# Kernel tuning notes

Hardware: AMD Instinct MI355X
Metric: run time of the kernel (lower is better)

The kernel has to match this reference:

```python
import jax, jax.numpy as jnp
import numpy as np

B, N, D_IN, D_HID, D_EDGE = 4, 256, 256, 256, 64


def setup_inputs() -> dict:
    key = jax.random.key(0)
    ks = jax.random.split(key, 8)
    s_in = 1.0 / np.sqrt(D_IN)
    s_h2 = 1.0 / np.sqrt(2 * D_HID)
    s_h = 1.0 / np.sqrt(D_HID)
    return {
        "x": jax.random.normal(ks[0], (B, N, D_IN), jnp.float32),
        "W_in": jax.random.uniform(ks[1], (D_HID, D_IN), jnp.float32, -s_in, s_in),
        "b_in": jax.random.uniform(ks[2], (D_HID,), jnp.float32, -s_in, s_in),
        "W1": jax.random.uniform(ks[3], (D_HID, 2 * D_HID), jnp.float32, -s_h2, s_h2),
        "b1": jax.random.uniform(ks[4], (D_HID,), jnp.float32, -s_h2, s_h2),
        "W2": jax.random.uniform(ks[5], (D_EDGE, D_HID), jnp.float32, -s_h, s_h),
        "b2": jax.random.uniform(ks[6], (D_EDGE,), jnp.float32, -s_h, s_h),
    }


def reference(x, W_in, b_in, W1, b1, W2, b2):
    # in_proj: [B,N,d_in] -> [B,N,h]
    h = jnp.einsum("bnd,hd->bnh", x, W_in) + b_in
    # cat([h_i, h_j]) @ W1 == h_i @ Wa + h_j @ Wb with W1 = [Wa | Wb].
    # Precompute the two N x h projections, then broadcast-add over the pair grid
    # instead of materializing the [B,N,N,2h] concat (same math, fused form).
    Wa, Wb = W1[:, :D_HID], W1[:, D_HID:]
    pa = jnp.einsum("bnh,gh->bng", h, Wa)  # [B,N,h]
    pb = jnp.einsum("bnh,gh->bng", h, Wb)  # [B,N,h]
    z = pa[:, :, None, :] + pb[:, None, :, :] + b1  # [B,N,N,h]
    z = z * jax.nn.sigmoid(z)  # Swish
    return jnp.einsum("bijh,eh->bije", z, W2) + b2  # [B,N,N,d_edge]
```

## Files before the change

kernel.cpp:

```cpp
#include <hip/hip_runtime.h>

#define DIN 256
#define DHID 256
#define DEDGE 64
#define GS 68

typedef float f32x4 __attribute__((ext_vector_type(4)));
typedef short s16x8 __attribute__((ext_vector_type(8)));
typedef unsigned int u32x4 __attribute__((ext_vector_type(4)));

__device__ __forceinline__ unsigned int cvtpk(float lo, float hi) {
    unsigned int r;
    asm("v_cvt_pk_bf16_f32 %0, %1, %2" : "=v"(r) : "v"(lo), "v"(hi));
    return r;
}

__global__ __launch_bounds__(256) void k_xh(
    const float* __restrict__ x, const float* __restrict__ Win,
    float* __restrict__ hp, const float* __restrict__ W2, s16x8* __restrict__ W2f)
{
    const int tid = threadIdx.x;
    if (blockIdx.z == 4) {
        if (tid < 32) {
            const int f = (((blockIdx.x << 2) + blockIdx.y) << 5) + tid;
            const int l15f = f & 15, qf = (f >> 4) & 3, ebf = (f >> 6) & 3, k0f = f >> 8;
            const int row = (ebf << 4) + l15f;
            const int col = (k0f << 5) + (qf << 3);
            const f32x4 w0 = *reinterpret_cast<const f32x4*>(&W2[row * DHID + col]);
            const f32x4 w1 = *reinterpret_cast<const f32x4*>(&W2[row * DHID + col + 4]);
            u32x4 wp;
            wp[0] = cvtpk(w0[0], w0[1]); wp[1] = cvtpk(w0[2], w0[3]);
            wp[2] = cvtpk(w1[0], w1[1]); wp[3] = cvtpk(w1[2], w1[3]);
            W2f[f] = __builtin_bit_cast(s16x8, wp);
        }
        return;
    }

    __shared__ float as[64 * GS];
    __shared__ float ws[64 * GS];
    const int m0 = blockIdx.x << 6, n0 = blockIdx.y << 6, k0 = blockIdx.z << 6;
    const int rr = tid >> 4;
    const int kk = (tid & 15) << 2;

#pragma unroll
    for (int it = 0; it < 4; ++it) {
        const int row = rr + (it << 4);
        *reinterpret_cast<f32x4*>(&as[row * GS + kk]) =
            *reinterpret_cast<const f32x4*>(&x[(m0 + row) * DIN + k0 + kk]);
        *reinterpret_cast<f32x4*>(&ws[row * GS + kk]) =
            *reinterpret_cast<const f32x4*>(&Win[(n0 + row) * DIN + k0 + kk]);
    }
    __syncthreads();

    const int tx = tid & 15, ty = tid >> 4;
    float acc[4][4] = {};
    for (int k = 0; k < 64; k += 4) {
        f32x4 av[4], wv[4];
#pragma unroll
        for (int r = 0; r < 4; ++r)
            av[r] = *reinterpret_cast<const f32x4*>(&as[(ty + (r << 4)) * GS + k]);
#pragma unroll
        for (int c = 0; c < 4; ++c)
            wv[c] = *reinterpret_cast<const f32x4*>(&ws[(tx + (c << 4)) * GS + k]);
#pragma unroll
        for (int r = 0; r < 4; ++r)
#pragma unroll
            for (int c = 0; c < 4; ++c)
                acc[r][c] += av[r][0]*wv[c][0] + av[r][1]*wv[c][1]
                           + av[r][2]*wv[c][2] + av[r][3]*wv[c][3];
    }
    float* dst = hp + ((size_t)blockIdx.z << 18);
#pragma unroll
    for (int r = 0; r < 4; ++r)
#pragma unroll
        for (int c = 0; c < 4; ++c)
            dst[(m0 + ty + (r << 4)) * DHID + n0 + tx + (c << 4)] = acc[r][c];
}

__global__ __launch_bounds__(256) void k_pab(
    const float* __restrict__ hp, const float* __restrict__ W1,
    const float* __restrict__ bin, float* __restrict__ pap, float* __restrict__ pbp)
{
    __shared__ float as[64 * GS];
    __shared__ float ws[64 * GS];
    const int m0 = blockIdx.x << 6;
    const int half = blockIdx.y >> 2;
    const int n0 = (blockIdx.y & 3) << 6;
    const int kc = blockIdx.z;
    const int tid = threadIdx.x;
    const int rr = tid >> 4, kk = (tid & 15) << 2;
    const int tx = tid & 15, ty = tid >> 4;

    float acc[4][4] = {};
    for (int kt = 0; kt < 2; ++kt) {
        const int k0 = (kc << 7) + (kt << 6);
        if (kt) __syncthreads();
#pragma unroll
        for (int it = 0; it < 4; ++it) {
            const int row = rr + (it << 4);
            const int aoff = (m0 + row) * DHID + k0 + kk;
            f32x4 av = *reinterpret_cast<const f32x4*>(&hp[aoff]);
            av += *reinterpret_cast<const f32x4*>(&hp[aoff + (1 << 18)]);
            av += *reinterpret_cast<const f32x4*>(&hp[aoff + (2 << 18)]);
            av += *reinterpret_cast<const f32x4*>(&hp[aoff + (3 << 18)]);
            av += *reinterpret_cast<const f32x4*>(&bin[k0 + kk]);
            *reinterpret_cast<f32x4*>(&as[row * GS + kk]) = av;
            *reinterpret_cast<f32x4*>(&ws[row * GS + kk]) =
                *reinterpret_cast<const f32x4*>(&W1[(n0 + row) * 512 + (half << 8) + k0 + kk]);
        }
        __syncthreads();

        for (int k = 0; k < 64; k += 4) {
            f32x4 av[4], wv[4];
#pragma unroll
            for (int r = 0; r < 4; ++r)
                av[r] = *reinterpret_cast<const f32x4*>(&as[(ty + (r << 4)) * GS + k]);
#pragma unroll
            for (int c = 0; c < 4; ++c)
                wv[c] = *reinterpret_cast<const f32x4*>(&ws[(tx + (c << 4)) * GS + k]);
#pragma unroll
            for (int r = 0; r < 4; ++r)
#pragma unroll
                for (int c = 0; c < 4; ++c)
                    acc[r][c] += av[r][0]*wv[c][0] + av[r][1]*wv[c][1]
                               + av[r][2]*wv[c][2] + av[r][3]*wv[c][3];
        }
    }
    float* dst = (half ? pbp : pap) + ((size_t)kc << 18);
#pragma unroll
    for (int r = 0; r < 4; ++r)
#pragma unroll
        for (int c = 0; c < 4; ++c)
            dst[(m0 + ty + (r << 4)) * DHID + n0 + tx + (c << 4)] = acc[r][c];
}

__global__ __launch_bounds__(256) void k_out(
    const float* __restrict__ pap, const float* __restrict__ pbp,
    const float* __restrict__ b1, const s16x8* __restrict__ W2f,
    const float* __restrict__ b2, float* __restrict__ out)
{
    __shared__ s16x8 w2s[2048];
    __shared__ float pab1[4][DHID];

    const int jb = blockIdx.x, i0 = blockIdx.y << 2, b = blockIdx.z;
    const int tid = threadIdx.x;

    {
        const float b1v = b1[tid];
#pragma unroll
        for (int ii = 0; ii < 4; ++ii) {
            const int off = (((b << 8) + i0 + ii) << 8) + tid;
            pab1[ii][tid] = pap[off] + pap[off + (1 << 18)] + b1v;
        }
    }
#pragma unroll
    for (int it = 0; it < 8; ++it)
        w2s[tid + (it << 8)] = W2f[tid + (it << 8)];
    __syncthreads();

    const int lane = tid & 63, wave = tid >> 6, quad = lane >> 4, l15 = lane & 15;
    const int j0 = (jb << 6) + (wave << 4);
    const int pboff = (((b << 8) + (j0 + l15)) << 8);
    const float* pbq0 = pbp + pboff;
    const float* pbq1 = pbp + (1 << 18) + pboff;

    f32x4 acc[4][4];
#pragma unroll
    for (int ii = 0; ii < 4; ++ii)
#pragma unroll
        for (int eb = 0; eb < 4; ++eb) acc[ii][eb] = (f32x4){0.f, 0.f, 0.f, 0.f};

    float b2v[4];
#pragma unroll
    for (int eb = 0; eb < 4; ++eb) b2v[eb] = b2[(eb << 4) + l15];

    for (int k0 = 0; k0 < 8; ++k0) {
        const int g = (k0 << 5) + (quad << 3);
        const f32x4 p0 = *reinterpret_cast<const f32x4*>(pbq0 + g)
                       + *reinterpret_cast<const f32x4*>(pbq1 + g);
        const f32x4 p1 = *reinterpret_cast<const f32x4*>(pbq0 + g + 4)
                       + *reinterpret_cast<const f32x4*>(pbq1 + g + 4);

        s16x8 bfrag[4];
#pragma unroll
        for (int eb = 0; eb < 4; ++eb)
            bfrag[eb] = w2s[((k0 << 2) + eb) * 64 + lane];

#pragma unroll
        for (int ii = 0; ii < 4; ++ii) {
            const f32x4 q0 = *reinterpret_cast<const f32x4*>(&pab1[ii][g]);
            const f32x4 q1 = *reinterpret_cast<const f32x4*>(&pab1[ii][g + 4]);
            float s[8];
#pragma unroll
            for (int jj = 0; jj < 4; ++jj) {
                const float z0 = q0[jj] + p0[jj];
                const float z1 = q1[jj] + p1[jj];
                const float e0 = __expf(-z0);
                const float e1 = __expf(-z1);
                s[jj]     = z0 * __builtin_amdgcn_rcpf(1.0f + e0);
                s[4 + jj] = z1 * __builtin_amdgcn_rcpf(1.0f + e1);
            }
            u32x4 ap;
            ap[0] = cvtpk(s[0], s[1]); ap[1] = cvtpk(s[2], s[3]);
            ap[2] = cvtpk(s[4], s[5]); ap[3] = cvtpk(s[6], s[7]);
            const s16x8 a = __builtin_bit_cast(s16x8, ap);
#pragma unroll
            for (int eb = 0; eb < 4; ++eb)
                acc[ii][eb] = __builtin_amdgcn_mfma_f32_16x16x32_bf16(a, bfrag[eb], acc[ii][eb], 0, 0, 0);
        }
    }

#pragma unroll
    for (int ii = 0; ii < 4; ++ii) {
        const int obase = (((((b << 8) + i0 + ii) << 8) + j0 + (quad << 2)) << 6) + l15;
#pragma unroll
        for (int eb = 0; eb < 4; ++eb) {
#pragma unroll
            for (int r = 0; r < 4; ++r)
                __builtin_nontemporal_store(acc[ii][eb][r] + b2v[eb],
                                            &out[obase + (r << 6) + (eb << 4)]);
        }
    }
}

extern "C" void kernel_launch(void* const* d_in, const int* in_sizes, int n_in,
                              void* d_out, int out_size, void* d_ws, size_t ws_size,
                              hipStream_t stream) {
    const float* x = 0; const float* Win = 0; const float* bin = 0;
    const float* W1 = 0; const float* b1 = 0; const float* W2 = 0; const float* b2 = 0;
    for (int idx = 0; idx < n_in; ++idx) {
        const int s = in_sizes[idx];
        if (s == 262144) x = (const float*)d_in[idx];
        else if (s == 131072) W1 = (const float*)d_in[idx];
        else if (s == 65536) Win = (const float*)d_in[idx];
        else if (s == 16384) W2 = (const float*)d_in[idx];
        else if (s == 64) b2 = (const float*)d_in[idx];
        else if (s == 256) { if (!bin) bin = (const float*)d_in[idx]; else b1 = (const float*)d_in[idx]; }
    }

    float* ws  = (float*)d_ws;
    float* hp  = ws;
    float* pap = hp + (4 << 18);
    float* pbp = pap + (2 << 18);
    float* w2f = pbp + (2 << 18);

    hipLaunchKernelGGL(k_xh,  dim3(16, 4, 5), dim3(256), 0, stream, x, Win, hp, W2, (s16x8*)w2f);
    hipLaunchKernelGGL(k_pab, dim3(16, 8, 2), dim3(256), 0, stream, hp, W1, bin, pap, pbp);
    hipLaunchKernelGGL(k_out, dim3(4, 64, 4), dim3(256), 0, stream,
                       pap, pbp, b1, (const s16x8*)w2f, b2, (float*)d_out);
}
```

Measured before the change: 125.8 us.

## Use split-bf16 MFMA for the pa/pb projection GEMM in k_pab

Replaces the scalar fp32 FMA tile GEMM in k_pab with bf16 MFMA 16x16x32 instructions. Operands are split into hi and lo bf16 parts and three MFMAs per tile (hi*hi, hi*lo, lo*hi) recover near-fp32 accuracy. Shared memory now holds four bf16 arrays with padded stride, and the K loop is processed in a single staged chunk. This trades extra conversion work and a small accuracy loss for matrix-core throughput on a kernel that is a small part of total time.

Result: faster. 120.9 us (-3.9%).

```diff
diff --git a/kernel.cpp b/kernel.cpp
--- a/kernel.cpp
+++ b/kernel.cpp
@@ -4,9 +4,11 @@
 #define DHID 256
 #define DEDGE 64
 #define GS 68
+#define BS 136
 
 typedef float f32x4 __attribute__((ext_vector_type(4)));
 typedef short s16x8 __attribute__((ext_vector_type(8)));
+typedef unsigned int u32x2 __attribute__((ext_vector_type(2)));
 typedef unsigned int u32x4 __attribute__((ext_vector_type(4)));
 
 __device__ __forceinline__ unsigned int cvtpk(float lo, float hi) {
@@ -81,57 +83,83 @@
     const float* __restrict__ hp, const float* __restrict__ W1,
     const float* __restrict__ bin, float* __restrict__ pap, float* __restrict__ pbp)
 {
-    __shared__ float as[64 * GS];
-    __shared__ float ws[64 * GS];
+    __shared__ unsigned short Ahi[64 * BS], Alo[64 * BS];
+    __shared__ unsigned short Bhi[64 * BS], Blo[64 * BS];
     const int m0 = blockIdx.x << 6;
     const int half = blockIdx.y >> 2;
     const int n0 = (blockIdx.y & 3) << 6;
     const int kc = blockIdx.z;
     const int tid = threadIdx.x;
-    const int rr = tid >> 4, kk = (tid & 15) << 2;
-    const int tx = tid & 15, ty = tid >> 4;
-
-    float acc[4][4] = {};
-    for (int kt = 0; kt < 2; ++kt) {
-        const int k0 = (kc << 7) + (kt << 6);
-        if (kt) __syncthreads();
-#pragma unroll
-        for (int it = 0; it < 4; ++it) {
-            const int row = rr + (it << 4);
-            const int aoff = (m0 + row) * DHID + k0 + kk;
-            f32x4 av = *reinterpret_cast<const f32x4*>(&hp[aoff]);
-            av += *reinterpret_cast<const f32x4*>(&hp[aoff + (1 << 18)]);
-            av += *reinterpret_cast<const f32x4*>(&hp[aoff + (2 << 18)]);
-            av += *reinterpret_cast<const f32x4*>(&hp[aoff + (3 << 18)]);
-            av += *reinterpret_cast<const f32x4*>(&bin[k0 + kk]);
-            *reinterpret_cast<f32x4*>(&as[row * GS + kk]) = av;
-            *reinterpret_cast<f32x4*>(&ws[row * GS + kk]) =
-                *reinterpret_cast<const f32x4*>(&W1[(n0 + row) * 512 + (half << 8) + k0 + kk]);
-        }
-        __syncthreads();
-
-        for (int k = 0; k < 64; k += 4) {
-            f32x4 av[4], wv[4];
-#pragma unroll
-            for (int r = 0; r < 4; ++r)
-                av[r] = *reinterpret_cast<const f32x4*>(&as[(ty + (r << 4)) * GS + k]);
-#pragma unroll
-            for (int c = 0; c < 4; ++c)
-                wv[c] = *reinterpret_cast<const f32x4*>(&ws[(tx + (c << 4)) * GS + k]);
-#pragma unroll
-            for (int r = 0; r < 4; ++r)
-#pragma unroll
-                for (int c = 0; c < 4; ++c)
-                    acc[r][c] += av[r][0]*wv[c][0] + av[r][1]*wv[c][1]
-                               + av[r][2]*wv[c][2] + av[r][3]*wv[c][3];
-        }
-    }
+    const int k0 = kc << 7;
+
+    const int srow = tid >> 2, sc0 = (tid & 3) << 2;
+    {
+        const float* hpA = hp + (m0 + srow) * DHID + k0 + sc0;
+        const float* w1B = W1 + (n0 + srow) * 512 + (half << 8) + k0 + sc0;
+        const float* binp = bin + k0 + sc0;
+#pragma unroll
+        for (int g2 = 0; g2 < 8; ++g2) {
+            const int c = g2 << 4;
+            f32x4 av = *reinterpret_cast<const f32x4*>(hpA + c);
+            av += *reinterpret_cast<const f32x4*>(hpA + c + (1 << 18));
+            av += *reinterpret_cast<const f32x4*>(hpA + c + (2 << 18));
+            av += *reinterpret_cast<const f32x4*>(hpA + c + (3 << 18));
+            av += *reinterpret_cast<const f32x4*>(binp + c);
+            unsigned int ah0 = cvtpk(av[0], av[1]), ah1 = cvtpk(av[2], av[3]);
+            f32x4 hf;
+            hf[0] = __builtin_bit_cast(float, ah0 << 16);
+            hf[1] = __builtin_bit_cast(float, ah0 & 0xffff0000u);
+            hf[2] = __builtin_bit_cast(float, ah1 << 16);
+            hf[3] = __builtin_bit_cast(float, ah1 & 0xffff0000u);
+            const f32x4 alo = av - hf;
+            const int la = srow * BS + sc0 + c;
+            *reinterpret_cast<u32x2*>(&Ahi[la]) = (u32x2){ah0, ah1};
+            *reinterpret_cast<u32x2*>(&Alo[la]) = (u32x2){cvtpk(alo[0], alo[1]), cvtpk(alo[2], alo[3])};
+
+            f32x4 bv = *reinterpret_cast<const f32x4*>(w1B + c);
+            unsigned int bh0 = cvtpk(bv[0], bv[1]), bh1 = cvtpk(bv[2], bv[3]);
+            f32x4 bf;
+            bf[0] = __builtin_bit_cast(float, bh0 << 16);
+            bf[1] = __builtin_bit_cast(float, bh0 & 0xffff0000u);
+            bf[2] = __builtin_bit_cast(float, bh1 << 16);
+            bf[3] = __builtin_bit_cast(float, bh1 & 0xffff0000u);
+            const f32x4 blo = bv - bf;
+            *reinterpret_cast<u32x2*>(&Bhi[la]) = (u32x2){bh0, bh1};
+            *reinterpret_cast<u32x2*>(&Blo[la]) = (u32x2){cvtpk(blo[0], blo[1]), cvtpk(blo[2], blo[3])};
+        }
+    }
+    __syncthreads();
+
+    const int lane = tid & 63, wave = tid >> 6, quad = lane >> 4, l15 = lane & 15;
+    const int arow = (wave << 4) + l15;
+
+    f32x4 acc[4];
+#pragma unroll
+    for (int nb = 0; nb < 4; ++nb) acc[nb] = (f32x4){0.f, 0.f, 0.f, 0.f};
+
+#pragma unroll
+    for (int ks = 0; ks < 4; ++ks) {
+        const int kcol = (ks << 5) + (quad << 3);
+        const s16x8 ahi = *reinterpret_cast<const s16x8*>(&Ahi[arow * BS + kcol]);
+        const s16x8 alo = *reinterpret_cast<const s16x8*>(&Alo[arow * BS + kcol]);
+#pragma unroll
+        for (int nb = 0; nb < 4; ++nb) {
+            const int brow = (nb << 4) + l15;
+            const s16x8 bhi = *reinterpret_cast<const s16x8*>(&Bhi[brow * BS + kcol]);
+            const s16x8 blo = *reinterpret_cast<const s16x8*>(&Blo[brow * BS + kcol]);
+            acc[nb] = __builtin_amdgcn_mfma_f32_16x16x32_bf16(ahi, bhi, acc[nb], 0, 0, 0);
+            acc[nb] = __builtin_amdgcn_mfma_f32_16x16x32_bf16(ahi, blo, acc[nb], 0, 0, 0);
+            acc[nb] = __builtin_amdgcn_mfma_f32_16x16x32_bf16(alo, bhi, acc[nb], 0, 0, 0);
+        }
+    }
+
     float* dst = (half ? pbp : pap) + ((size_t)kc << 18);
-#pragma unroll
-    for (int r = 0; r < 4; ++r)
-#pragma unroll
-        for (int c = 0; c < 4; ++c)
-            dst[(m0 + ty + (r << 4)) * DHID + n0 + tx + (c << 4)] = acc[r][c];
+    const int mrow = m0 + (wave << 4) + (quad << 2);
+#pragma unroll
+    for (int nb = 0; nb < 4; ++nb)
+#pragma unroll
+        for (int r = 0; r < 4; ++r)
+            dst[(mrow + r) * DHID + n0 + (nb << 4) + l15] = acc[nb][r];
 }
 
 __global__ __launch_bounds__(256) void k_out(
```
